# Performance work log

Hardware: AMD Instinct MI355X
Metric: run time of the kernel (lower is better)

## Reference

```python
import jax, jax.numpy as jnp
import numpy as np
from jax import lax

BIT_SIZE = 8
ES_SIZE = 1


def posit_quantize(x, nbits=BIT_SIZE, es=ES_SIZE):
    """Round x to the nearest posit(nbits, es) representable value (round-to-nearest
    of the fraction given the regime/exponent-dependent fraction width)."""
    sign = jnp.sign(x)
    a = jnp.abs(x)
    safe = jnp.where(a > 0, a, jnp.ones_like(a))
    logx = jnp.floor(jnp.log2(safe))            # binade exponent
    ipow = 2 ** es                               # 2^es, python int
    k = jnp.floor(logx / ipow)                   # regime value
    regime_len = jnp.where(k >= 0, k + 2, -k + 1)
    fbits = jnp.clip(nbits - 1 - regime_len - es, 0, 23)  # fraction bits left
    scale = jnp.exp2(logx)
    frac = safe / scale                          # in [1, 2)
    step = jnp.exp2(fbits)
    q = jnp.round(frac * step) / step * scale
    maxpos = jnp.float32(2.0 ** ((nbits - 2) * ipow))
    minpos = jnp.float32(2.0 ** (-(nbits - 2) * ipow))
    q = jnp.clip(q, minpos, maxpos)
    return jnp.where(a > 0, sign * q, jnp.zeros_like(x))


def pq(x):
    # straight-through quantizer (forward value is exact posit rounding)
    return x + lax.stop_gradient(posit_quantize(x) - x)


def conv2d(x, w):  # NCHW, OIHW, valid, stride 1
    return lax.conv_general_dilated(x, w, (1, 1), 'VALID',
                                    dimension_numbers=('NCHW', 'OIHW', 'NCHW'))


def maxpool2(x):
    return lax.reduce_window(x, -jnp.inf, lax.max,
                             (1, 1, 2, 2), (1, 1, 2, 2), 'VALID')


def setup_inputs() -> dict:
    key = jax.random.key(0)
    ks = jax.random.split(key, 9)
    B = 4096
    x = jax.random.normal(ks[0], (B, 1, 28, 28), jnp.float32)
    def init_w(k, shape, fan_in):
        bound = 1.0 / np.sqrt(fan_in)
        return jax.random.uniform(k, shape, jnp.float32, -bound, bound)
    conv1_w = init_w(ks[1], (32, 1, 3, 3), 1 * 9)
    conv1_b = init_w(ks[2], (32,), 1 * 9)
    conv2_w = init_w(ks[3], (64, 32, 3, 3), 32 * 9)
    conv2_b = init_w(ks[4], (64,), 32 * 9)
    fc1_w = init_w(ks[5], (128, 12 * 12 * 64), 12 * 12 * 64)
    fc1_b = init_w(ks[6], (128,), 12 * 12 * 64)
    fc2_w = init_w(ks[7], (10, 128), 128)
    fc2_b = init_w(ks[8], (10,), 128)
    return dict(x=x, conv1_w=conv1_w, conv1_b=conv1_b, conv2_w=conv2_w,
                conv2_b=conv2_b, fc1_w=fc1_w, fc1_b=fc1_b,
                fc2_w=fc2_w, fc2_b=fc2_b)


def reference(x, conv1_w, conv1_b, conv2_w, conv2_b, fc1_w, fc1_b, fc2_w, fc2_b):
    # PositizedConv2d: posit-quantize activations and weights, conv in fp32, add bias
    h = conv2d(pq(x), pq(conv1_w)) + conv1_b[None, :, None, None]   # [B,32,26,26]
    h = jax.nn.relu(h)
    h = conv2d(pq(h), pq(conv2_w)) + conv2_b[None, :, None, None]   # [B,64,24,24]
    h = jax.nn.relu(h)
    h = maxpool2(h)                                                  # [B,64,12,12]
    # dropout layers are identity in eval mode
    h = h.reshape(-1, 12 * 12 * 64)
    h = jax.nn.relu(jnp.dot(pq(h), pq(fc1_w).T) + fc1_b)             # [B,128]
    out = jnp.dot(pq(h), pq(fc2_w).T) + fc2_b                        # [B,10]
    return out
```

## Files before the change

### kernel.cpp

```cpp
#include <hip/hip_runtime.h>

using u16 = unsigned short;
using u32 = unsigned int;
typedef __attribute__((ext_vector_type(8))) short bf16x8;
typedef __attribute__((ext_vector_type(4))) float f32x4;

__device__ __forceinline__ float posit_q(float x) {
    float a = __builtin_fabsf(x);
    u32 u = __float_as_uint(a);
    int logx = (int)(u >> 23) - 127;
    logx = logx < -60 ? -60 : (logx > 60 ? 60 : logx);
    float frac = __uint_as_float((u & 0x007fffffu) | 0x3f800000u);
    int k = logx >> 1;
    int rl = (k >= 0) ? (k + 2) : (1 - k);
    int fb = 6 - rl; fb = fb < 0 ? 0 : fb;
    float step = (float)(1 << fb);
    float q = rintf(frac * step) * __uint_as_float((u32)(127 + logx - fb) << 23);
    q = fminf(fmaxf(q, 0x1p-12f), 0x1p12f);
    return (a > 0.0f) ? copysignf(q, x) : 0.0f;
}

__device__ __forceinline__ float b2f(u16 v) { return __uint_as_float((u32)v << 16); }
__device__ __forceinline__ u16 f2b(float f) { return (u16)(__float_as_uint(f) >> 16); }

__device__ __forceinline__ void lut_init(int tid, float* lut) {
    if (tid < 256) {
        int e = tid - 127;
        float m = 0.f;
        if (e >= -12 && e <= 12) {
            int k = e >> 1;
            int rl = max(k + 2, 1 - k);
            int fb = max(6 - rl, 0);
            m = __uint_as_float((u32)(150 + e - fb) << 23) * 1.5f;
        }
        lut[tid] = m;
    }
}
__device__ __forceinline__ u32 pq_pos_raw(float x, const float* __restrict__ lut) {
    u32 u = __float_as_uint(x);
    float c = lut[u >> 23];
    float q = (x + c) - c;
    q = fminf(fmaxf(q, 0x1p-12f), 0x1p12f);
    return u == 0u ? 0u : __float_as_uint(q);
}

__global__ __launch_bounds__(256) void prep_kernel(
    const float* __restrict__ w1, const float* __restrict__ w2,
    const float* __restrict__ fw2,
    float* __restrict__ w1q, u16* __restrict__ w2frag, float* __restrict__ fc2wq) {
    int i = blockIdx.x * 256 + threadIdx.x;
    if (i < 288)  w1q[i]   = posit_q(w1[i]);
    if (i < 1280) fc2wq[i] = posit_q(fw2[i]);
    if (i < 18432) {
        int e = i & 7, lane = (i >> 3) & 63, c9 = i >> 9;
        int kc = c9 % 9, nt = c9 / 9;
        int n = nt * 16 + (lane & 15);
        int ci = ((lane >> 4) << 3) + e;
        w2frag[i] = f2b(posit_q(w2[n * 288 + ci * 9 + kc]));
    }
}

#define PLS 5416
__global__ __launch_bounds__(512, 4) void conv_fused_kernel(
    const float* __restrict__ x, const float* __restrict__ w1q, const float* __restrict__ b1,
    const u16* __restrict__ w2frag, const float* __restrict__ b2,
    const float* __restrict__ fw1, u16* __restrict__ fc1wq, u16* __restrict__ pooled) {
    __shared__ __align__(16) float sX[784];
    __shared__ __align__(16) u16 sH1[4 * PLS];
    __shared__ float sLut[256];
    int img = blockIdx.x, tid = threadIdx.x;
    int wave = tid >> 6, lane = tid & 63;
    int col = lane & 15, quad = lane >> 4;

    lut_init(tid, sLut);

    for (int i = tid; i < 784; i += 512) sX[i] = posit_q(x[(size_t)img * 784 + i]);
    if (tid < 288) {
        int j = img * 288 + tid;
        int e = j & 7, ln = (j >> 3) & 63, c = j >> 9;
        int kk = c % 288, nt = c / 288;
        int n = nt * 16 + (ln & 15);
        int k = kk * 32 + ((ln >> 4) << 3) + e;
        fc1wq[j] = f2b(posit_q(fw1[(size_t)n * 9216 + k]));
    }

    int ocp = tid & 15;
    float wreg[18];
#pragma unroll
    for (int j = 0; j < 18; ++j) wreg[j] = w1q[ocp * 18 + j];
    float bias0 = b1[ocp * 2], bias1 = b1[ocp * 2 + 1];

    __syncthreads();

    int pgrp = tid >> 4;
    u16* h1dst = &sH1[(ocp >> 2) * PLS + 2 * (ocp & 3)];
    for (int it = 0; it < 6; ++it) {
        int q = it * 32 + pgrp;
        if (q < 169) {
            int py = q / 13, px = q - py * 13;
            const float* base = &sX[2 * py * 28 + 2 * px];
            float in4[4][4];
#pragma unroll
            for (int r = 0; r < 4; ++r) {
                float2 lo = *(const float2*)(base + r * 28);
                float2 hi = *(const float2*)(base + r * 28 + 2);
                in4[r][0] = lo.x; in4[r][1] = lo.y; in4[r][2] = hi.x; in4[r][3] = hi.y;
            }
#pragma unroll
            for (int dy = 0; dy < 2; ++dy)
#pragma unroll
            for (int dx = 0; dx < 2; ++dx) {
                float a0 = bias0, a1 = bias1;
#pragma unroll
                for (int j = 0; j < 9; ++j) {
                    float v = in4[dy + j / 3][dx + j % 3];
                    a0 = fmaf(wreg[j], v, a0);
                    a1 = fmaf(wreg[9 + j], v, a1);
                }
                u32 r0 = pq_pos_raw(fmaxf(a0, 0.f), sLut);
                u32 r1 = pq_pos_raw(fmaxf(a1, 0.f), sLut);
                int p = (2 * py + dy) * 26 + 2 * px + dx;
                *(u32*)&h1dst[p * 8] = (r0 >> 16) | (r1 & 0xFFFF0000u);
            }
        }
    }

    __syncthreads();
    int npair = wave & 1, mq = wave >> 1;
    bf16x8 bfrag[2][9];
#pragma unroll
    for (int j = 0; j < 2; ++j)
#pragma unroll
        for (int kc = 0; kc < 9; ++kc)
            bfrag[j][kc] = *(const bf16x8*)(w2frag + (((npair * 2 + j) * 9 + kc) * 64 + lane) * 8);
    float cb0 = b2[(npair * 2) * 16 + col];
    float cb1 = b2[(npair * 2 + 1) * 16 + col];
    u16* gout0 = pooled + (size_t)img * 9216 + ((npair * 2) * 16 + col) * 144;
    u16* gout1 = pooled + (size_t)img * 9216 + ((npair * 2 + 1) * 16 + col) * 144;
    const u16* aplane = &sH1[quad * PLS];
    int wsl = col >> 2;
    int wswz = ((wsl & 1) << 1) | (wsl >> 1);
    int qswz = ((quad & 1) << 1) | (quad >> 1);
    int wi = col & 3;

    for (int t = 0; t < 9; ++t) {
        int mt = mq * 9 + t;
        int pp = mt * 4 + wswz;
        int py = pp / 12, px_ = pp - py * 12;
        int oh = 2 * py + (wi >> 1), ow = 2 * px_ + (wi & 1);
        const u16* ap = aplane + (oh * 26 + ow) * 8;
        f32x4 acc0 = {0.f, 0.f, 0.f, 0.f}, acc1 = {0.f, 0.f, 0.f, 0.f};
#pragma unroll
        for (int kc = 0; kc < 9; ++kc) {
            int kh = kc / 3, kw = kc - kh * 3;
            bf16x8 af = *(const bf16x8*)(ap + (kh * 26 + kw) * 8);
            acc0 = __builtin_amdgcn_mfma_f32_16x16x32_bf16(af, bfrag[0][kc], acc0, 0, 0, 0);
            acc1 = __builtin_amdgcn_mfma_f32_16x16x32_bf16(af, bfrag[1][kc], acc1, 0, 0, 0);
        }
        float mx0 = fmaxf(fmaxf(acc0[0], acc0[1]), fmaxf(acc0[2], acc0[3]));
        float mx1 = fmaxf(fmaxf(acc1[0], acc1[1]), fmaxf(acc1[2], acc1[3]));
        gout0[mt * 4 + qswz] = (u16)(pq_pos_raw(fmaxf(mx0 + cb0, 0.f), sLut) >> 16);
        gout1[mt * 4 + qswz] = (u16)(pq_pos_raw(fmaxf(mx1 + cb1, 0.f), sLut) >> 16);
    }
}

__global__ __launch_bounds__(512, 2) void fc1_part_kernel(const u16* __restrict__ pooled,
    const u16* __restrict__ fc1wqF, float* __restrict__ part) {
    __shared__ __align__(16) float sAcc[8448];
    int blk = blockIdx.x, tid = threadIdx.x;
    int mbp = blk >> 2, ks = blk & 3;
    int wave = tid >> 6, lane = tid & 63;
    int row = lane & 15, quad = lane >> 4;

    const bf16x8* bbase = (const bf16x8*)fc1wqF + (size_t)(ks * 72 + wave * 9) * 64 + lane;
    const u16* abase0 = pooled + (size_t)(mbp * 32 + row) * 9216 + ks * 2304 + wave * 288 + quad * 8;
    const u16* abase1 = abase0 + (size_t)16 * 9216;
    f32x4 acc[2][8];
#pragma unroll
    for (int mi = 0; mi < 2; ++mi)
#pragma unroll
        for (int nt = 0; nt < 8; ++nt) acc[mi][nt] = f32x4{0.f, 0.f, 0.f, 0.f};
    bf16x8 a0n = *(const bf16x8*)(abase0);
    bf16x8 a1n = *(const bf16x8*)(abase1);
#pragma unroll 1
    for (int k2 = 0; k2 < 9; ++k2) {
        bf16x8 a0 = a0n, a1 = a1n;
        if (k2 < 8) {
            a0n = *(const bf16x8*)(abase0 + (k2 + 1) * 32);
            a1n = *(const bf16x8*)(abase1 + (k2 + 1) * 32);
        }
#pragma unroll
        for (int nt = 0; nt < 8; ++nt) {
            bf16x8 b = bbase[((size_t)nt * 288 + k2) * 64];
            acc[0][nt] = __builtin_amdgcn_mfma_f32_16x16x32_bf16(a0, b, acc[0][nt], 0, 0, 0);
            acc[1][nt] = __builtin_amdgcn_mfma_f32_16x16x32_bf16(a1, b, acc[1][nt], 0, 0, 0);
        }
    }
#pragma unroll
    for (int mi = 0; mi < 2; ++mi) {
        if (mi) __syncthreads();
        if (wave < 4) {
#pragma unroll
            for (int nt = 0; nt < 8; ++nt)
#pragma unroll
                for (int r = 0; r < 4; ++r)
                    sAcc[wave * 2112 + (quad * 4 + r) * 132 + nt * 16 + row] = acc[mi][nt][r];
        }
        __syncthreads();
        if (wave >= 4) {
#pragma unroll
            for (int nt = 0; nt < 8; ++nt)
#pragma unroll
                for (int r = 0; r < 4; ++r)
                    sAcc[(wave - 4) * 2112 + (quad * 4 + r) * 132 + nt * 16 + row] += acc[mi][nt][r];
        }
        __syncthreads();
        size_t pbase = ((size_t)((mbp * 2 + mi) * 4 + ks)) * 2048;
        for (int e = tid; e < 2048; e += 512) {
            int o = (e >> 7) * 132 + (e & 127);
            part[pbase + e] = sAcc[o] + sAcc[2112 + o] + sAcc[4224 + o] + sAcc[6336 + o];
        }
    }
}

__global__ __launch_bounds__(256) void fc2_red_kernel(const float* __restrict__ part,
    const float* __restrict__ fc1b, const float* __restrict__ fc2wq,
    const float* __restrict__ fc2b, float* __restrict__ out) {
    __shared__ __align__(16) u16 sFc1[2048];
    __shared__ float sW2[1280];
    __shared__ float sB2[16];
    __shared__ float sLut[256];
    int mb = blockIdx.x, tid = threadIdx.x;
    lut_init(tid, sLut);
    for (int i = tid; i < 1280; i += 256) sW2[i] = fc2wq[i];
    if (tid < 10) sB2[tid] = fc2b[tid];
    __syncthreads();
    const float* pb = part + (size_t)mb * 4 * 2048;
    for (int e = tid; e < 2048; e += 256) {
        float s = pb[e] + pb[2048 + e] + pb[4096 + e] + pb[6144 + e];
        sFc1[e] = (u16)(pq_pos_raw(fmaxf(s + fc1b[e & 127], 0.f), sLut) >> 16);
    }
    __syncthreads();
    if (tid < 160) {
        int il = tid / 10, oc = tid - il * 10;
        float s = sB2[oc];
        const u16* hp = &sFc1[il * 128];
        const float* wp = &sW2[oc * 128];
#pragma unroll
        for (int k = 0; k < 128; ++k) s = fmaf(b2f(hp[k]), wp[k], s);
        out[(size_t)(mb * 16 + il) * 10 + oc] = s;
    }
}

extern "C" void kernel_launch(void* const* d_in, const int* in_sizes, int n_in,
                              void* d_out, int out_size, void* d_ws, size_t ws_size,
                              hipStream_t stream) {
    const float* x    = (const float*)d_in[0];
    const float* w1   = (const float*)d_in[1];
    const float* b1   = (const float*)d_in[2];
    const float* w2   = (const float*)d_in[3];
    const float* b2   = (const float*)d_in[4];
    const float* fw1  = (const float*)d_in[5];
    const float* fb1  = (const float*)d_in[6];
    const float* fw2  = (const float*)d_in[7];
    const float* fb2  = (const float*)d_in[8];
    float* out = (float*)d_out;

    char* ws = (char*)d_ws;
    float* w1q     = (float*)(ws + 0);
    float* fc2wq   = (float*)(ws + 1280);
    u16*   w2frag  = (u16*)(ws + 6400);
    u16*   fc1wqF  = (u16*)(ws + 43520);
    u16*   pooled  = (u16*)(ws + 4762112);
    float* part    = (float*)(ws + 80259584);

    prep_kernel<<<72, 256, 0, stream>>>(w1, w2, fw2, w1q, w2frag, fc2wq);
    conv_fused_kernel<<<4096, 512, 0, stream>>>(x, w1q, b1, w2frag, b2, fw1, fc1wqF, pooled);
    fc1_part_kernel<<<512, 512, 0, stream>>>(pooled, fc1wqF, part);
    fc2_red_kernel<<<256, 256, 0, stream>>>(part, fb1, fc2wq, fb2, out);
}
```

Baseline: 221.2 us.

## Retile conv2 MFMA loop so each wave covers all output channels

```diff
diff --git a/kernel.cpp b/kernel.cpp
--- a/kernel.cpp
+++ b/kernel.cpp
@@ -60,8 +60,53 @@
     }
 }
 
+template<int TB>
+__device__ __forceinline__ void conv2_tblock(
+    int mt0, int wswz, int qswz, int wi, int lane,
+    const u16* __restrict__ aplane, const u16* __restrict__ w2frag,
+    const float (&cb)[4], u16* const (&gout)[4], const float* __restrict__ sLut) {
+    int aoff[TB];
+#pragma unroll
+    for (int t = 0; t < TB; ++t) {
+        int pp = (mt0 + t) * 4 + wswz;
+        int py = pp / 12, px_ = pp - py * 12;
+        int oh = 2 * py + (wi >> 1), ow = 2 * px_ + (wi & 1);
+        aoff[t] = (oh * 26 + ow) * 8;
+    }
+    f32x4 acc[TB][4];
+#pragma unroll
+    for (int t = 0; t < TB; ++t)
+#pragma unroll
+        for (int j = 0; j < 4; ++j) acc[t][j] = f32x4{0.f, 0.f, 0.f, 0.f};
+#pragma unroll
+    for (int kc = 0; kc < 9; ++kc) {
+        int kh = kc / 3, kw = kc - kh * 3;
+        bf16x8 bf[4];
+#pragma unroll
+        for (int j = 0; j < 4; ++j)
+            bf[j] = *(const bf16x8*)(w2frag + ((j * 9 + kc) * 64 + lane) * 8);
+#pragma unroll
+        for (int t = 0; t < TB; ++t) {
+            bf16x8 af = *(const bf16x8*)(aplane + aoff[t] + (kh * 26 + kw) * 8);
+#pragma unroll
+            for (int j = 0; j < 4; ++j)
+                acc[t][j] = __builtin_amdgcn_mfma_f32_16x16x32_bf16(af, bf[j], acc[t][j], 0, 0, 0);
+        }
+    }
+#pragma unroll
+    for (int t = 0; t < TB; ++t) {
+        int mt = mt0 + t;
+#pragma unroll
+        for (int j = 0; j < 4; ++j) {
+            float mx = fmaxf(fmaxf(acc[t][j][0], acc[t][j][1]), fmaxf(acc[t][j][2], acc[t][j][3]));
+            gout[j][mt * 4 + qswz] = (u16)(pq_pos_raw(fmaxf(mx + cb[j], 0.f), sLut) >> 16);
+        }
+    }
+}
+
 #define PLS 5416
-__global__ __launch_bounds__(512, 4) void conv_fused_kernel(
+__global__ __launch_bounds__(512) __attribute__((amdgpu_waves_per_eu(4, 4)))
+void conv_fused_kernel(
     const float* __restrict__ x, const float* __restrict__ w1q, const float* __restrict__ b1,
     const u16* __restrict__ w2frag, const float* __restrict__ b2,
     const float* __restrict__ fw1, u16* __restrict__ fc1wq, u16* __restrict__ pooled) {
@@ -126,41 +171,28 @@
     }
 
     __syncthreads();
-    int npair = wave & 1, mq = wave >> 1;
-    bf16x8 bfrag[2][9];
-#pragma unroll
-    for (int j = 0; j < 2; ++j)
-#pragma unroll
-        for (int kc = 0; kc < 9; ++kc)
-            bfrag[j][kc] = *(const bf16x8*)(w2frag + (((npair * 2 + j) * 9 + kc) * 64 + lane) * 8);
-    float cb0 = b2[(npair * 2) * 16 + col];
-    float cb1 = b2[(npair * 2 + 1) * 16 + col];
-    u16* gout0 = pooled + (size_t)img * 9216 + ((npair * 2) * 16 + col) * 144;
-    u16* gout1 = pooled + (size_t)img * 9216 + ((npair * 2 + 1) * 16 + col) * 144;
+
+    float cb[4];
+    u16* gout[4];
+#pragma unroll
+    for (int j = 0; j < 4; ++j) {
+        cb[j] = b2[j * 16 + col];
+        gout[j] = pooled + (size_t)img * 9216 + (j * 16 + col) * 144;
+    }
     const u16* aplane = &sH1[quad * PLS];
     int wsl = col >> 2;
     int wswz = ((wsl & 1) << 1) | (wsl >> 1);
     int qswz = ((quad & 1) << 1) | (quad >> 1);
     int wi = col & 3;
 
-    for (int t = 0; t < 9; ++t) {
-        int mt = mq * 9 + t;
-        int pp = mt * 4 + wswz;
-        int py = pp / 12, px_ = pp - py * 12;
-        int oh = 2 * py + (wi >> 1), ow = 2 * px_ + (wi & 1);
-        const u16* ap = aplane + (oh * 26 + ow) * 8;
-        f32x4 acc0 = {0.f, 0.f, 0.f, 0.f}, acc1 = {0.f, 0.f, 0.f, 0.f};
-#pragma unroll
-        for (int kc = 0; kc < 9; ++kc) {
-            int kh = kc / 3, kw = kc - kh * 3;
-            bf16x8 af = *(const bf16x8*)(ap + (kh * 26 + kw) * 8);
-            acc0 = __builtin_amdgcn_mfma_f32_16x16x32_bf16(af, bfrag[0][kc], acc0, 0, 0, 0);
-            acc1 = __builtin_amdgcn_mfma_f32_16x16x32_bf16(af, bfrag[1][kc], acc1, 0, 0, 0);
-        }
-        float mx0 = fmaxf(fmaxf(acc0[0], acc0[1]), fmaxf(acc0[2], acc0[3]));
-        float mx1 = fmaxf(fmaxf(acc1[0], acc1[1]), fmaxf(acc1[2], acc1[3]));
-        gout0[mt * 4 + qswz] = (u16)(pq_pos_raw(fmaxf(mx0 + cb0, 0.f), sLut) >> 16);
-        gout1[mt * 4 + qswz] = (u16)(pq_pos_raw(fmaxf(mx1 + cb1, 0.f), sLut) >> 16);
+    if (wave < 4) {
+        int base = wave * 5;
+        conv2_tblock<3>(base,     wswz, qswz, wi, lane, aplane, w2frag, cb, gout, sLut);
+        conv2_tblock<2>(base + 3, wswz, qswz, wi, lane, aplane, w2frag, cb, gout, sLut);
+    } else {
+        int base = 20 + (wave - 4) * 4;
+        conv2_tblock<2>(base,     wswz, qswz, wi, lane, aplane, w2frag, cb, gout, sLut);
+        conv2_tblock<2>(base + 2, wswz, qswz, wi, lane, aplane, w2frag, cb, gout, sLut);
     }
 }
 
```

After: 258.5 us. 1.17x slower.
